# Kernel optimization log

Measured on AMD Instinct MI355X. Metric: run time of the kernel, lower is better.

The kernel has to match this reference:

```python
import jax, jax.numpy as jnp
import numpy as np


def _mamba_branch(xz, conv_w, conv_b, xproj_w, dtproj_w, dtproj_b, A_log, Dp):
    # xz: (b, l, 2*d_inner)
    d_inner, d_state = A_log.shape
    dt_rank = dtproj_w.shape[1]
    k = conv_w.shape[-1]
    x, z = jnp.split(xz, 2, axis=-1)                      # (b, l, d_inner) each
    # depthwise causal conv over the sequence dim (torch pads d_conv-1 then trims to L)
    xc = jax.lax.conv_general_dilated(
        x.transpose(0, 2, 1), conv_w, (1,), [(k - 1, 0)],
        feature_group_count=d_inner,
        dimension_numbers=('NCH', 'OIH', 'NCH'))
    x = jax.nn.silu((xc + conv_b[None, :, None]).transpose(0, 2, 1))  # (b, l, d)
    dbl = x @ xproj_w.T                                   # (b, l, dt_rank + 2*n)
    dt, Bs, Cs = jnp.split(dbl, [dt_rank, dt_rank + d_state], axis=-1)
    delta = jax.nn.softplus(dt @ dtproj_w.T + dtproj_b)   # (b, l, d)
    A = -jnp.exp(A_log)                                   # (d, n), always negative

    def step(h, inp):
        d_t, B_t, u_t, C_t = inp                          # (b,d),(b,n),(b,d),(b,n)
        h = jnp.exp(d_t[..., None] * A) * h + (d_t * u_t)[..., None] * B_t[:, None, :]
        return h, jnp.einsum('bdn,bn->bd', h, C_t)

    h0 = jnp.zeros((x.shape[0], d_inner, d_state), x.dtype)
    _, ys = jax.lax.scan(step, h0,
                         (delta.transpose(1, 0, 2), Bs.transpose(1, 0, 2),
                          x.transpose(1, 0, 2), Cs.transpose(1, 0, 2)))
    y = ys.transpose(1, 0, 2) + x * Dp                    # (b, l, d)
    return y * jax.nn.silu(z)


def setup_inputs() -> dict:
    key = jax.random.key(0)
    ks = jax.random.split(key, 12)
    dim, d_state, d_conv, expand = 256, 16, 4, 2
    d_inner = expand * dim
    dt_rank = dim // 16
    s = 0.02
    r = lambda k, shp: s * jax.random.normal(k, shp, jnp.float32)
    A_init = jnp.log(jnp.tile(jnp.arange(1, d_state + 1, dtype=jnp.float32), (d_inner, 1)))
    dt_bias = jnp.log(jnp.expm1(0.01 * jnp.ones((d_inner,), jnp.float32)))
    return {
        'x': jax.random.normal(ks[0], (8, dim, 64, 64), jnp.float32),
        'ln_w': jnp.ones((dim,), jnp.float32),
        'ln_b': jnp.zeros((dim,), jnp.float32),
        'in_proj_w': r(ks[1], (2 * d_inner, dim)),
        'conv1d_w': r(ks[2], (d_inner, 1, d_conv)),
        'conv1d_b': jnp.zeros((d_inner,), jnp.float32),
        'x_proj_w': r(ks[3], (dt_rank + 2 * d_state, d_inner)),
        'dt_proj_w': r(ks[4], (d_inner, dt_rank)),
        'dt_proj_b': dt_bias,
        'A_log': A_init,
        'D': jnp.ones((d_inner,), jnp.float32),
        'conv1d_b_w': r(ks[5], (d_inner, 1, d_conv)),
        'conv1d_b_b': jnp.zeros((d_inner,), jnp.float32),
        'x_proj_b_w': r(ks[6], (dt_rank + 2 * d_state, d_inner)),
        'dt_proj_b_w': r(ks[7], (d_inner, dt_rank)),
        'dt_proj_b_b': dt_bias,
        'A_b_log': A_init,
        'D_b': jnp.ones((d_inner,), jnp.float32),
        'out_proj_w': r(ks[8], (dim, d_inner)),
    }


def reference(x, ln_w, ln_b, in_proj_w, conv1d_w, conv1d_b, x_proj_w, dt_proj_w,
              dt_proj_b, A_log, D, conv1d_b_w, conv1d_b_b, x_proj_b_w,
              dt_proj_b_w, dt_proj_b_b, A_b_log, D_b, out_proj_w):
    B, C, H, W = x.shape
    xf = x.reshape(B, C, H * W).transpose(0, 2, 1)        # (b, l, c)
    mu = jnp.mean(xf, -1, keepdims=True)
    var = jnp.mean((xf - mu) ** 2, -1, keepdims=True)
    xn = (xf - mu) / jnp.sqrt(var + 1e-5) * ln_w + ln_b   # LayerNorm(dim)
    xz = xn @ in_proj_w.T                                 # (b, l, 2*d_inner)
    y_f = _mamba_branch(xz, conv1d_w, conv1d_b, x_proj_w, dt_proj_w,
                        dt_proj_b, A_log, D)
    y_b = _mamba_branch(xz[:, ::-1, :], conv1d_b_w, conv1d_b_b, x_proj_b_w,
                        dt_proj_b_w, dt_proj_b_b, A_b_log, D_b)[:, ::-1, :]
    out = (y_f + y_b) @ out_proj_w.T                      # (b, l, c)
    return out.transpose(0, 2, 1).reshape(B, C, H, W)
```

## Files before the change

### kernel.cpp

```cpp
#include <hip/hip_runtime.h>
#include <cstdint>
#include <cstddef>

#define L_SEQ   4096
#define NBATCH  8
#define NDIM    256
#define DIN     512
#define NSTATE  16
#define NC_CHUNKS 32
#define CLEN    (L_SEQ / NC_CHUNKS)
#define BLROWS  (NBATCH * L_SEQ)

typedef unsigned short u16;
typedef __attribute__((ext_vector_type(8))) short short8;
typedef __attribute__((ext_vector_type(4))) float f32x4;

#define LOG2E 1.44269504088896340736f

__device__ __forceinline__ u16 f2bf(float f) {
  unsigned u = __float_as_uint(f);
  return (u16)((u + 0x7FFFu + ((u >> 16) & 1u)) >> 16);
}
__device__ __forceinline__ float bf2f(u16 v) {
  return __uint_as_float(((unsigned)v) << 16);
}
__device__ __forceinline__ float exp2fast(float x) {
#if __has_builtin(__builtin_amdgcn_exp2f)
  return __builtin_amdgcn_exp2f(x);
#else
  return exp2f(x);
#endif
}
__device__ __forceinline__ float sigmoid_(float x) {
  return 1.0f / (1.0f + exp2fast(-x * LOG2E));
}
__device__ __forceinline__ float silu_(float x) { return x * sigmoid_(x); }
__device__ __forceinline__ float softplus_(float x) {
  return (x > 15.f) ? x : __logf(1.0f + exp2fast(x * LOG2E));
}

__global__ __launch_bounds__(256) void k_prep(
    const float* __restrict__ in_w, const float* __restrict__ xp_f,
    const float* __restrict__ xp_b, const float* __restrict__ out_w,
    const float* __restrict__ Alog_f, const float* __restrict__ Alog_b,
    u16* __restrict__ wb_in, u16* __restrict__ wb_xp, u16* __restrict__ wb_cat,
    float* __restrict__ a2) {
  int i = blockIdx.x * 256 + threadIdx.x;
  if (i < 1024 * 256) wb_in[i] = f2bf(in_w[i]);
  if (i < 2 * 48 * 512) {
    int d = i / (48 * 512), r = i % (48 * 512);
    wb_xp[i] = f2bf((d ? xp_b : xp_f)[r]);
  }
  if (i < 256 * 1024) {
    int c = i >> 10, k = i & 1023;
    wb_cat[i] = f2bf(out_w[c * 512 + (k & 511)]);
  }
  if (i < 2 * 8192) {
    int d = i >> 13, r = i & 8191;
    a2[i] = -__expf((d ? Alog_b : Alog_f)[r]) * LOG2E;
  }
}

__global__ __launch_bounds__(256) void k_ln(
    const float* __restrict__ x, const float* __restrict__ w,
    const float* __restrict__ bb, u16* __restrict__ xn) {
  __shared__ float tile[256][65];
  __shared__ float red[2][4][64];
  __shared__ float mu_s[64], rs_s[64];
  int b = blockIdx.y, l0 = blockIdx.x * 64;
  int t = threadIdx.x, lane = t & 63, r = t >> 6;
  const float* xb = x + (size_t)b * 256 * L_SEQ;
  for (int cc = 0; cc < 64; ++cc) {
    int c = cc * 4 + r;
    tile[c][lane] = xb[(size_t)c * L_SEQ + l0 + lane];
  }
  __syncthreads();
  float s = 0.f, sq = 0.f;
  for (int c = r * 64; c < r * 64 + 64; ++c) {
    float v = tile[c][lane];
    s += v; sq += v * v;
  }
  red[0][r][lane] = s; red[1][r][lane] = sq;
  __syncthreads();
  if (t < 64) {
    float S = red[0][0][t] + red[0][1][t] + red[0][2][t] + red[0][3][t];
    float Q = red[1][0][t] + red[1][1][t] + red[1][2][t] + red[1][3][t];
    float mu = S * (1.f / 256.f);
    float var = Q * (1.f / 256.f) - mu * mu;
    mu_s[t] = mu;
    rs_s[t] = rsqrtf(var + 1e-5f);
  }
  __syncthreads();
  float wc = w[t], bc = bb[t];
  for (int l = 0; l < 64; ++l) {
    float v = (tile[t][l] - mu_s[l]) * rs_s[l] * wc + bc;
    xn[((size_t)b * L_SEQ + l0 + l) * 256 + t] = f2bf(v);
  }
}

__global__ __launch_bounds__(256) void k_gemm_in(
    const u16* __restrict__ A, const u16* __restrict__ Bm,
    u16* __restrict__ xout, u16* __restrict__ zout) {
  __shared__ u16 lA[128 * 32], lB[128 * 32];
  int mt = blockIdx.x, nt = blockIdx.y;
  int t = threadIdx.x, lane = t & 63, wid = t >> 6;
  int wr = wid >> 1, wc = wid & 1;
  f32x4 acc[4][4] = {};
  const u16* Ab = A + (size_t)mt * 128 * 256;
  const u16* Bb = Bm + (size_t)nt * 128 * 256;
  for (int kt = 0; kt < 8; ++kt) {
    int k0 = kt * 32;
    __syncthreads();
#pragma unroll
    for (int i = 0; i < 2; ++i) {
      int lin = i * 256 + t, row = lin >> 2, kc = lin & 3;
      *(short8*)&lA[lin * 8] = *(const short8*)&Ab[row * 256 + k0 + kc * 8];
      *(short8*)&lB[lin * 8] = *(const short8*)&Bb[row * 256 + k0 + kc * 8];
    }
    __syncthreads();
    short8 av[4], bv[4];
#pragma unroll
    for (int i = 0; i < 4; ++i)
      av[i] = *(const short8*)&lA[(wr * 64 + i * 16 + (lane & 15)) * 32 + (lane >> 4) * 8];
#pragma unroll
    for (int j = 0; j < 4; ++j)
      bv[j] = *(const short8*)&lB[(wc * 64 + j * 16 + (lane & 15)) * 32 + (lane >> 4) * 8];
#pragma unroll
    for (int i = 0; i < 4; ++i)
#pragma unroll
      for (int j = 0; j < 4; ++j)
        acc[i][j] = __builtin_amdgcn_mfma_f32_16x16x32_bf16(av[i], bv[j], acc[i][j], 0, 0, 0);
  }
  int colbase = nt * 128 + wc * 64;
  u16* dst = (colbase < 512) ? xout : zout;
  int cadj = (colbase < 512) ? colbase : colbase - 512;
  size_t rowbase = (size_t)mt * 128 + wr * 64;
#pragma unroll
  for (int i = 0; i < 4; ++i)
#pragma unroll
    for (int j = 0; j < 4; ++j) {
      int c = cadj + j * 16 + (lane & 15);
      size_t rr = rowbase + i * 16 + ((lane >> 4) << 2);
#pragma unroll
      for (int ii = 0; ii < 4; ++ii)
        dst[(rr + ii) * 512 + c] = f2bf(acc[i][j][ii]);
    }
}

__global__ __launch_bounds__(512) void k_conv(
    const u16* __restrict__ xbuf,
    const float* __restrict__ cw_f, const float* __restrict__ cb_f,
    const float* __restrict__ cw_b, const float* __restrict__ cb_b,
    u16* __restrict__ xconv_bf) {
  int d = threadIdx.x;
  int b = blockIdx.y, dir = blockIdx.z;
  int t0 = blockIdx.x * 64;
  const float* cw = (dir ? cw_b : cw_f) + d * 4;
  float w0 = cw[0], w1 = cw[1], w2 = cw[2], w3 = cw[3];
  float bias = (dir ? cb_b : cb_f)[d];
  const u16* xb = xbuf + (size_t)b * L_SEQ * 512 + d;
  u16* ob = xconv_bf + ((size_t)dir * BLROWS + (size_t)b * L_SEQ) * 512 + d;
  float tp0 = 0.f, tp1 = 0.f, tp2 = 0.f;
  if (t0 >= 1) tp2 = bf2f(xb[(size_t)(dir ? (L_SEQ - t0) : (t0 - 1)) * 512]);
  if (t0 >= 2) tp1 = bf2f(xb[(size_t)(dir ? (L_SEQ + 1 - t0) : (t0 - 2)) * 512]);
  if (t0 >= 3) tp0 = bf2f(xb[(size_t)(dir ? (L_SEQ + 2 - t0) : (t0 - 3)) * 512]);
#pragma unroll 4
  for (int tt = t0; tt < t0 + 64; ++tt) {
    int px = dir ? (L_SEQ - 1 - tt) : tt;
    float xin = bf2f(xb[(size_t)px * 512]);
    float u = bias + w0 * tp0 + w1 * tp1 + w2 * tp2 + w3 * xin;
    ob[(size_t)tt * 512] = f2bf(silu_(u));
    tp0 = tp1; tp1 = tp2; tp2 = xin;
  }
}

__global__ __launch_bounds__(256) void k_gemm_xp(
    const u16* __restrict__ xc, const u16* __restrict__ wxp,
    float* __restrict__ dbl) {
  __shared__ u16 lA[128 * 32], lB[48 * 32];
  int mt = blockIdx.x, dir = blockIdx.y;
  int t = threadIdx.x, lane = t & 63, wid = t >> 6;
  const u16* Ab = xc + ((size_t)dir * BLROWS + (size_t)mt * 128) * 512;
  const u16* Bb = wxp + (size_t)dir * 48 * 512;
  float* Ob = dbl + ((size_t)dir * BLROWS + (size_t)mt * 128) * 48;
  f32x4 acc[2][3] = {};
  for (int kt = 0; kt < 16; ++kt) {
    int k0 = kt * 32;
    __syncthreads();
#pragma unroll
    for (int i = 0; i < 2; ++i) {
      int lin = i * 256 + t, row = lin >> 2, kc = lin & 3;
      *(short8*)&lA[lin * 8] = *(const short8*)&Ab[row * 512 + k0 + kc * 8];
    }
    if (t < 192) {
      int row = t >> 2, kc = t & 3;
      *(short8*)&lB[t * 8] = *(const short8*)&Bb[row * 512 + k0 + kc * 8];
    }
    __syncthreads();
    short8 av[2], bv[3];
#pragma unroll
    for (int i = 0; i < 2; ++i)
      av[i] = *(const short8*)&lA[(wid * 32 + i * 16 + (lane & 15)) * 32 + (lane >> 4) * 8];
#pragma unroll
    for (int j = 0; j < 3; ++j)
      bv[j] = *(const short8*)&lB[(j * 16 + (lane & 15)) * 32 + (lane >> 4) * 8];
#pragma unroll
    for (int i = 0; i < 2; ++i)
#pragma unroll
      for (int j = 0; j < 3; ++j)
        acc[i][j] = __builtin_amdgcn_mfma_f32_16x16x32_bf16(av[i], bv[j], acc[i][j], 0, 0, 0);
  }
#pragma unroll
  for (int i = 0; i < 2; ++i)
#pragma unroll
    for (int j = 0; j < 3; ++j) {
      int c = j * 16 + (lane & 15);
      int rr = wid * 32 + i * 16 + ((lane >> 4) << 2);
#pragma unroll
      for (int ii = 0; ii < 4; ++ii)
        Ob[(size_t)(rr + ii) * 48 + c] = acc[i][j][ii];
    }
}

__global__ __launch_bounds__(512, 4) void k_scanA(
    const u16* __restrict__ xbuf, const float* __restrict__ dbl,
    const float* __restrict__ a2buf,
    const float* __restrict__ cw_f, const float* __restrict__ cb_f,
    const float* __restrict__ cw_b, const float* __restrict__ cb_b,
    const float* __restrict__ dtw_f, const float* __restrict__ dtb_f,
    const float* __restrict__ dtw_b, const float* __restrict__ dtb_b,
    float* __restrict__ Pb, float* __restrict__ Hf) {
  int chunk = blockIdx.x, b = blockIdx.y, dir = blockIdx.z;
  int d = threadIdx.x;
  f32x4 a2r[4], w3r[4];
  const f32x4* A2 = (const f32x4*)(a2buf + dir * 8192 + (size_t)d * 16);
  const f32x4* dtw = (const f32x4*)((dir ? dtw_b : dtw_f) + (size_t)d * 16);
#pragma unroll
  for (int q = 0; q < 4; ++q) { a2r[q] = A2[q]; w3r[q] = dtw[q]; }
  const float* cw = (dir ? cw_b : cw_f) + d * 4;
  float w0 = cw[0], w1 = cw[1], w2 = cw[2], w3 = cw[3];
  float cbias = (dir ? cb_b : cb_f)[d];
  float dtbias = (dir ? dtb_b : dtb_f)[d];
  const u16* xb = xbuf + (size_t)b * L_SEQ * 512 + d;
  const float* dbr = dbl + ((size_t)dir * BLROWS + (size_t)b * L_SEQ) * 48;
  int t0 = chunk * CLEN;
  float tp0 = 0.f, tp1 = 0.f, tp2 = 0.f;
  if (t0 >= 1) tp2 = bf2f(xb[(size_t)(dir ? (L_SEQ - t0) : (t0 - 1)) * 512]);
  if (t0 >= 2) tp1 = bf2f(xb[(size_t)(dir ? (L_SEQ + 1 - t0) : (t0 - 2)) * 512]);
  if (t0 >= 3) tp0 = bf2f(xb[(size_t)(dir ? (L_SEQ + 2 - t0) : (t0 - 3)) * 512]);
  f32x4 h[4] = {};
  float S = 0.f;
  for (int tt = t0; tt < t0 + CLEN; ++tt) {
    int px = dir ? (L_SEQ - 1 - tt) : tt;
    float xin = bf2f(xb[(size_t)px * 512]);
    float u = silu_(cbias + w0 * tp0 + w1 * tp1 + w2 * tp2 + w3 * xin);
    tp0 = tp1; tp1 = tp2; tp2 = xin;
    const f32x4* row4 = (const f32x4*)(dbr + (size_t)tt * 48);
    float v0 = 0.f, v1 = 0.f, v2 = 0.f, v3 = 0.f;
#pragma unroll
    for (int q = 0; q < 4; ++q) {
      f32x4 dq = row4[q];
      v0 = fmaf(dq[0], w3r[q][0], v0); v1 = fmaf(dq[1], w3r[q][1], v1);
      v2 = fmaf(dq[2], w3r[q][2], v2); v3 = fmaf(dq[3], w3r[q][3], v3);
    }
    float delta = softplus_(dtbias + ((v0 + v1) + (v2 + v3)));
    S += delta;
    float du = delta * u;
#pragma unroll
    for (int q = 0; q < 4; ++q) {
      f32x4 Bv = row4[4 + q];
#pragma unroll
      for (int j = 0; j < 4; ++j)
        h[q][j] = fmaf(exp2fast(delta * a2r[q][j]), h[q][j], du * Bv[j]);
    }
  }
  size_t base = (((size_t)dir * NBATCH + b) * NC_CHUNKS + chunk) * 8192 + (size_t)d * 16;
#pragma unroll
  for (int q = 0; q < 4; ++q) {
    *(f32x4*)&Hf[base + q * 4] = h[q];
    f32x4 pv;
#pragma unroll
    for (int j = 0; j < 4; ++j) pv[j] = exp2fast(S * a2r[q][j]);
    *(f32x4*)&Pb[base + q * 4] = pv;
  }
}

__global__ __launch_bounds__(512) void k_scanB(
    const float* __restrict__ P, const float* __restrict__ Hf,
    float* __restrict__ Hi) {
  int dir = blockIdx.z, b = blockIdx.y;
  int j = blockIdx.x * 512 + threadIdx.x;
  size_t base0 = (((size_t)dir * NBATCH + b) * NC_CHUNKS) * 8192 + j;
  float h = 0.f;
  for (int c = 0; c < NC_CHUNKS; ++c) {
    size_t idx = base0 + (size_t)c * 8192;
    Hi[idx] = h;
    h = P[idx] * h + Hf[idx];
  }
}

__global__ __launch_bounds__(512, 4) void k_scanC(
    const u16* __restrict__ xbuf, const u16* __restrict__ zbuf,
    const float* __restrict__ dbl, const float* __restrict__ a2buf,
    const float* __restrict__ cw_f, const float* __restrict__ cb_f,
    const float* __restrict__ cw_b, const float* __restrict__ cb_b,
    const float* __restrict__ dtw_f, const float* __restrict__ dtb_f,
    const float* __restrict__ dtw_b, const float* __restrict__ dtb_b,
    const float* __restrict__ D_f, const float* __restrict__ D_b,
    const float* __restrict__ Hi, u16* __restrict__ ycat) {
  int chunk = blockIdx.x, b = blockIdx.y, dir = blockIdx.z;
  int d = threadIdx.x;
  f32x4 a2r[4], w3r[4];
  const f32x4* A2 = (const f32x4*)(a2buf + dir * 8192 + (size_t)d * 16);
  const f32x4* dtw = (const f32x4*)((dir ? dtw_b : dtw_f) + (size_t)d * 16);
#pragma unroll
  for (int q = 0; q < 4; ++q) { a2r[q] = A2[q]; w3r[q] = dtw[q]; }
  const float* cw = (dir ? cw_b : cw_f) + d * 4;
  float w0 = cw[0], w1 = cw[1], w2 = cw[2], w3 = cw[3];
  float cbias = (dir ? cb_b : cb_f)[d];
  float dtbias = (dir ? dtb_b : dtb_f)[d];
  float Dd = (dir ? D_b : D_f)[d];
  const u16* xb = xbuf + (size_t)b * L_SEQ * 512 + d;
  const u16* zb = zbuf + (size_t)b * L_SEQ * 512 + d;
  const float* dbr = dbl + ((size_t)dir * BLROWS + (size_t)b * L_SEQ) * 48;
  u16* yb = ycat + (size_t)b * L_SEQ * 1024 + dir * 512 + d;
  int t0 = chunk * CLEN;
  float tp0 = 0.f, tp1 = 0.f, tp2 = 0.f;
  if (t0 >= 1) tp2 = bf2f(xb[(size_t)(dir ? (L_SEQ - t0) : (t0 - 1)) * 512]);
  if (t0 >= 2) tp1 = bf2f(xb[(size_t)(dir ? (L_SEQ + 1 - t0) : (t0 - 2)) * 512]);
  if (t0 >= 3) tp0 = bf2f(xb[(size_t)(dir ? (L_SEQ + 2 - t0) : (t0 - 3)) * 512]);
  f32x4 h[4];
  size_t hbase = (((size_t)dir * NBATCH + b) * NC_CHUNKS + chunk) * 8192 + (size_t)d * 16;
#pragma unroll
  for (int q = 0; q < 4; ++q) h[q] = *(const f32x4*)&Hi[hbase + q * 4];
  for (int tt = t0; tt < t0 + CLEN; ++tt) {
    int px = dir ? (L_SEQ - 1 - tt) : tt;
    float xin = bf2f(xb[(size_t)px * 512]);
    float u = silu_(cbias + w0 * tp0 + w1 * tp1 + w2 * tp2 + w3 * xin);
    tp0 = tp1; tp1 = tp2; tp2 = xin;
    const f32x4* row4 = (const f32x4*)(dbr + (size_t)tt * 48);
    float v0 = 0.f, v1 = 0.f, v2 = 0.f, v3 = 0.f;
#pragma unroll
    for (int q = 0; q < 4; ++q) {
      f32x4 dq = row4[q];
      v0 = fmaf(dq[0], w3r[q][0], v0); v1 = fmaf(dq[1], w3r[q][1], v1);
      v2 = fmaf(dq[2], w3r[q][2], v2); v3 = fmaf(dq[3], w3r[q][3], v3);
    }
    float delta = softplus_(dtbias + ((v0 + v1) + (v2 + v3)));
    float du = delta * u;
    f32x4 yv = {0.f, 0.f, 0.f, 0.f};
#pragma unroll
    for (int q = 0; q < 4; ++q) {
      f32x4 Bv = row4[4 + q];
      f32x4 Cv = row4[8 + q];
#pragma unroll
      for (int j = 0; j < 4; ++j) {
        h[q][j] = fmaf(exp2fast(delta * a2r[q][j]), h[q][j], du * Bv[j]);
        yv[j] = fmaf(h[q][j], Cv[j], yv[j]);
      }
    }
    float y = ((yv[0] + yv[1]) + (yv[2] + yv[3])) + u * Dd;
    float z = bf2f(zb[(size_t)px * 512]);
    yb[(size_t)px * 1024] = f2bf(y * silu_(z));
  }
}

__global__ __launch_bounds__(256) void k_gemm_out(
    const u16* __restrict__ A, const u16* __restrict__ Bm,
    float* __restrict__ out) {
  __shared__ u16 lA[128 * 32], lB[128 * 32];
  int mt = blockIdx.x, nt = blockIdx.y;
  int t = threadIdx.x, lane = t & 63, wid = t >> 6;
  int wr = wid >> 1, wc = wid & 1;
  f32x4 acc[4][4] = {};
  const u16* Ab = A + (size_t)mt * 128 * 1024;
  const u16* Bb = Bm + (size_t)nt * 128 * 1024;
  for (int kt = 0; kt < 32; ++kt) {
    int k0 = kt * 32;
    __syncthreads();
#pragma unroll
    for (int i = 0; i < 2; ++i) {
      int lin = i * 256 + t, row = lin >> 2, kc = lin & 3;
      *(short8*)&lA[lin * 8] = *(const short8*)&Ab[(size_t)row * 1024 + k0 + kc * 8];
      *(short8*)&lB[lin * 8] = *(const short8*)&Bb[(size_t)row * 1024 + k0 + kc * 8];
    }
    __syncthreads();
    short8 av[4], bv[4];
#pragma unroll
    for (int i = 0; i < 4; ++i)
      av[i] = *(const short8*)&lA[(wr * 64 + i * 16 + (lane & 15)) * 32 + (lane >> 4) * 8];
#pragma unroll
    for (int j = 0; j < 4; ++j)
      bv[j] = *(const short8*)&lB[(wc * 64 + j * 16 + (lane & 15)) * 32 + (lane >> 4) * 8];
#pragma unroll
    for (int i = 0; i < 4; ++i)
#pragma unroll
      for (int j = 0; j < 4; ++j)
        acc[i][j] = __builtin_amdgcn_mfma_f32_16x16x32_bf16(av[i], bv[j], acc[i][j], 0, 0, 0);
  }
#pragma unroll
  for (int i = 0; i < 4; ++i)
#pragma unroll
    for (int j = 0; j < 4; ++j) {
      int c = nt * 128 + wc * 64 + j * 16 + (lane & 15);
      int r0 = mt * 128 + wr * 64 + i * 16 + ((lane >> 4) << 2);
      int b = r0 >> 12, l0 = r0 & 4095;
      float4 val;
      val.x = acc[i][j][0]; val.y = acc[i][j][1];
      val.z = acc[i][j][2]; val.w = acc[i][j][3];
      *(float4*)&out[((size_t)b * 256 + c) * 4096 + l0] = val;
    }
}

extern "C" void kernel_launch(void* const* d_in, const int* in_sizes, int n_in,
                              void* d_out, int out_size, void* d_ws, size_t ws_size,
                              hipStream_t stream) {
  (void)in_sizes; (void)n_in; (void)out_size; (void)ws_size;
  const float* x      = (const float*)d_in[0];
  const float* ln_w   = (const float*)d_in[1];
  const float* ln_b   = (const float*)d_in[2];
  const float* in_w   = (const float*)d_in[3];
  const float* cw_f   = (const float*)d_in[4];
  const float* cb_f   = (const float*)d_in[5];
  const float* xp_f   = (const float*)d_in[6];
  const float* dtw_f  = (const float*)d_in[7];
  const float* dtb_f  = (const float*)d_in[8];
  const float* Alog_f = (const float*)d_in[9];
  const float* D_f    = (const float*)d_in[10];
  const float* cw_b   = (const float*)d_in[11];
  const float* cb_b   = (const float*)d_in[12];
  const float* xp_b   = (const float*)d_in[13];
  const float* dtw_b  = (const float*)d_in[14];
  const float* dtb_b  = (const float*)d_in[15];
  const float* Alog_b = (const float*)d_in[16];
  const float* D_b    = (const float*)d_in[17];
  const float* out_w  = (const float*)d_in[18];

  char* ws = (char*)d_ws;
  size_t off = 0;
  auto alloc = [&](size_t bytes) -> void* {
    void* p = ws + off;
    off += (bytes + 255) & ~(size_t)255;
    return p;
  };
  u16*   xn_bf  = (u16*)  alloc((size_t)BLROWS * 256 * 2);
  u16*   wb_in  = (u16*)  alloc((size_t)1024 * 256 * 2);
  u16*   wb_xp  = (u16*)  alloc((size_t)2 * 48 * 512 * 2);
  u16*   wb_cat = (u16*)  alloc((size_t)256 * 1024 * 2);
  float* a2buf  = (float*)alloc((size_t)2 * 8192 * 4);
  u16*   xbuf   = (u16*)  alloc((size_t)BLROWS * 512 * 2);
  u16*   zbuf   = (u16*)  alloc((size_t)BLROWS * 512 * 2);
  u16*   xconv  = (u16*)  alloc((size_t)2 * BLROWS * 512 * 2);
  float* dblb   = (float*)alloc((size_t)2 * BLROWS * 48 * 4);
  float* Hfbuf  = (float*)alloc((size_t)2 * NBATCH * NC_CHUNKS * 8192 * 4);
  float* Hibuf  = (float*)alloc((size_t)2 * NBATCH * NC_CHUNKS * 8192 * 4);
  float* Pbuf   = (float*)xn_bf;
  u16*   ycat   = xconv;

  hipLaunchKernelGGL(k_prep, dim3(1024), dim3(256), 0, stream,
                     in_w, xp_f, xp_b, out_w, Alog_f, Alog_b,
                     wb_in, wb_xp, wb_cat, a2buf);
  hipLaunchKernelGGL(k_ln, dim3(L_SEQ / 64, NBATCH), dim3(256), 0, stream,
                     x, ln_w, ln_b, xn_bf);
  hipLaunchKernelGGL(k_gemm_in, dim3(BLROWS / 128, 8), dim3(256), 0, stream,
                     xn_bf, wb_in, xbuf, zbuf);
  hipLaunchKernelGGL(k_conv, dim3(L_SEQ / 64, NBATCH, 2), dim3(512), 0, stream,
                     xbuf, cw_f, cb_f, cw_b, cb_b, xconv);
  hipLaunchKernelGGL(k_gemm_xp, dim3(BLROWS / 128, 2), dim3(256), 0, stream,
                     xconv, wb_xp, dblb);
  hipLaunchKernelGGL(k_scanA, dim3(NC_CHUNKS, NBATCH, 2), dim3(512), 0, stream,
                     xbuf, dblb, a2buf, cw_f, cb_f, cw_b, cb_b,
                     dtw_f, dtb_f, dtw_b, dtb_b, Pbuf, Hfbuf);
  hipLaunchKernelGGL(k_scanB, dim3(16, NBATCH, 2), dim3(512), 0, stream,
                     Pbuf, Hfbuf, Hibuf);
  hipLaunchKernelGGL(k_scanC, dim3(NC_CHUNKS, NBATCH, 2), dim3(512), 0, stream,
                     xbuf, zbuf, dblb, a2buf, cw_f, cb_f, cw_b, cb_b,
                     dtw_f, dtb_f, dtw_b, dtb_b, D_f, D_b, Hibuf, ycat);
  hipLaunchKernelGGL(k_gemm_out, dim3(BLROWS / 128, 2), dim3(256), 0, stream,
                     ycat, wb_cat, (float*)d_out);
}
```

Measured before the change: 621.1 us.

## Split scan state across four lanes per channel and reuse precomputed conv output

The chunked scan kernels now give each channel's 16 SSM states to four lanes instead of one thread. The dt projection and the C-weighted output are reduced with cross-lane shuffles, and the grid grows fourfold. The depthwise conv and SiLU are no longer recomputed in the scan; the scan reads the conv buffer already produced for the x-projection GEMM. The output ycat gets its own buffer because xconv must stay alive. This trades more threads and shuffle traffic for less per-thread serial work, fewer registers and higher occupancy.

```diff
diff --git a/kernel.cpp b/kernel.cpp
--- a/kernel.cpp
+++ b/kernel.cpp
@@ -223,66 +223,48 @@
 }
 
 __global__ __launch_bounds__(512, 4) void k_scanA(
-    const u16* __restrict__ xbuf, const float* __restrict__ dbl,
+    const u16* __restrict__ uconv, const float* __restrict__ dbl,
     const float* __restrict__ a2buf,
-    const float* __restrict__ cw_f, const float* __restrict__ cb_f,
-    const float* __restrict__ cw_b, const float* __restrict__ cb_b,
     const float* __restrict__ dtw_f, const float* __restrict__ dtb_f,
     const float* __restrict__ dtw_b, const float* __restrict__ dtb_b,
     float* __restrict__ Pb, float* __restrict__ Hf) {
-  int chunk = blockIdx.x, b = blockIdx.y, dir = blockIdx.z;
-  int d = threadIdx.x;
-  f32x4 a2r[4], w3r[4];
-  const f32x4* A2 = (const f32x4*)(a2buf + dir * 8192 + (size_t)d * 16);
-  const f32x4* dtw = (const f32x4*)((dir ? dtw_b : dtw_f) + (size_t)d * 16);
-#pragma unroll
-  for (int q = 0; q < 4; ++q) { a2r[q] = A2[q]; w3r[q] = dtw[q]; }
-  const float* cw = (dir ? cw_b : cw_f) + d * 4;
-  float w0 = cw[0], w1 = cw[1], w2 = cw[2], w3 = cw[3];
-  float cbias = (dir ? cb_b : cb_f)[d];
+  int chunk = blockIdx.x >> 2, cb = blockIdx.x & 3;
+  int b = blockIdx.y, dir = blockIdx.z;
+  int t = threadIdx.x, wid = t >> 6, lane = t & 63;
+  int ch = lane & 15, grp = lane >> 4;
+  int d = cb * 128 + wid * 16 + ch;
+  f32x4 a2r = *(const f32x4*)(a2buf + dir * 8192 + (size_t)d * 16 + grp * 4);
+  f32x4 w3r = *(const f32x4*)((dir ? dtw_b : dtw_f) + (size_t)d * 16 + grp * 4);
   float dtbias = (dir ? dtb_b : dtb_f)[d];
-  const u16* xb = xbuf + (size_t)b * L_SEQ * 512 + d;
-  const float* dbr = dbl + ((size_t)dir * BLROWS + (size_t)b * L_SEQ) * 48;
+  const u16* ub = uconv + ((size_t)dir * BLROWS + (size_t)b * L_SEQ) * 512 + d;
+  const float* dbr = dbl + ((size_t)dir * BLROWS + (size_t)b * L_SEQ) * 48 + grp * 4;
   int t0 = chunk * CLEN;
-  float tp0 = 0.f, tp1 = 0.f, tp2 = 0.f;
-  if (t0 >= 1) tp2 = bf2f(xb[(size_t)(dir ? (L_SEQ - t0) : (t0 - 1)) * 512]);
-  if (t0 >= 2) tp1 = bf2f(xb[(size_t)(dir ? (L_SEQ + 1 - t0) : (t0 - 2)) * 512]);
-  if (t0 >= 3) tp0 = bf2f(xb[(size_t)(dir ? (L_SEQ + 2 - t0) : (t0 - 3)) * 512]);
-  f32x4 h[4] = {};
+  f32x4 h = {0.f, 0.f, 0.f, 0.f};
   float S = 0.f;
   for (int tt = t0; tt < t0 + CLEN; ++tt) {
-    int px = dir ? (L_SEQ - 1 - tt) : tt;
-    float xin = bf2f(xb[(size_t)px * 512]);
-    float u = silu_(cbias + w0 * tp0 + w1 * tp1 + w2 * tp2 + w3 * xin);
-    tp0 = tp1; tp1 = tp2; tp2 = xin;
-    const f32x4* row4 = (const f32x4*)(dbr + (size_t)tt * 48);
-    float v0 = 0.f, v1 = 0.f, v2 = 0.f, v3 = 0.f;
-#pragma unroll
-    for (int q = 0; q < 4; ++q) {
-      f32x4 dq = row4[q];
-      v0 = fmaf(dq[0], w3r[q][0], v0); v1 = fmaf(dq[1], w3r[q][1], v1);
-      v2 = fmaf(dq[2], w3r[q][2], v2); v3 = fmaf(dq[3], w3r[q][3], v3);
-    }
-    float delta = softplus_(dtbias + ((v0 + v1) + (v2 + v3)));
+    float u = bf2f(ub[(size_t)tt * 512]);
+    f32x4 dq = *(const f32x4*)(dbr + (size_t)tt * 48);
+    f32x4 Bv = *(const f32x4*)(dbr + (size_t)tt * 48 + 16);
+    float part = dq[0] * w3r[0];
+    part = fmaf(dq[1], w3r[1], part);
+    part = fmaf(dq[2], w3r[2], part);
+    part = fmaf(dq[3], w3r[3], part);
+    part += __shfl_xor(part, 16);
+    part += __shfl_xor(part, 32);
+    float delta = softplus_(dtbias + part);
     S += delta;
     float du = delta * u;
 #pragma unroll
-    for (int q = 0; q < 4; ++q) {
-      f32x4 Bv = row4[4 + q];
-#pragma unroll
-      for (int j = 0; j < 4; ++j)
-        h[q][j] = fmaf(exp2fast(delta * a2r[q][j]), h[q][j], du * Bv[j]);
-    }
-  }
-  size_t base = (((size_t)dir * NBATCH + b) * NC_CHUNKS + chunk) * 8192 + (size_t)d * 16;
-#pragma unroll
-  for (int q = 0; q < 4; ++q) {
-    *(f32x4*)&Hf[base + q * 4] = h[q];
-    f32x4 pv;
-#pragma unroll
-    for (int j = 0; j < 4; ++j) pv[j] = exp2fast(S * a2r[q][j]);
-    *(f32x4*)&Pb[base + q * 4] = pv;
-  }
+    for (int j = 0; j < 4; ++j)
+      h[j] = fmaf(exp2fast(delta * a2r[j]), h[j], du * Bv[j]);
+  }
+  size_t base = (((size_t)dir * NBATCH + b) * NC_CHUNKS + chunk) * 8192
+              + (size_t)d * 16 + grp * 4;
+  *(f32x4*)&Hf[base] = h;
+  f32x4 pv;
+#pragma unroll
+  for (int j = 0; j < 4; ++j) pv[j] = exp2fast(S * a2r[j]);
+  *(f32x4*)&Pb[base] = pv;
 }
 
 __global__ __launch_bounds__(512) void k_scanB(
@@ -300,68 +282,56 @@
 }
 
 __global__ __launch_bounds__(512, 4) void k_scanC(
-    const u16* __restrict__ xbuf, const u16* __restrict__ zbuf,
+    const u16* __restrict__ uconv, const u16* __restrict__ zbuf,
     const float* __restrict__ dbl, const float* __restrict__ a2buf,
-    const float* __restrict__ cw_f, const float* __restrict__ cb_f,
-    const float* __restrict__ cw_b, const float* __restrict__ cb_b,
     const float* __restrict__ dtw_f, const float* __restrict__ dtb_f,
     const float* __restrict__ dtw_b, const float* __restrict__ dtb_b,
     const float* __restrict__ D_f, const float* __restrict__ D_b,
     const float* __restrict__ Hi, u16* __restrict__ ycat) {
-  int chunk = blockIdx.x, b = blockIdx.y, dir = blockIdx.z;
-  int d = threadIdx.x;
-  f32x4 a2r[4], w3r[4];
-  const f32x4* A2 = (const f32x4*)(a2buf + dir * 8192 + (size_t)d * 16);
-  const f32x4* dtw = (const f32x4*)((dir ? dtw_b : dtw_f) + (size_t)d * 16);
-#pragma unroll
-  for (int q = 0; q < 4; ++q) { a2r[q] = A2[q]; w3r[q] = dtw[q]; }
-  const float* cw = (dir ? cw_b : cw_f) + d * 4;
-  float w0 = cw[0], w1 = cw[1], w2 = cw[2], w3 = cw[3];
-  float cbias = (dir ? cb_b : cb_f)[d];
+  int chunk = blockIdx.x >> 2, cb = blockIdx.x & 3;
+  int b = blockIdx.y, dir = blockIdx.z;
+  int t = threadIdx.x, wid = t >> 6, lane = t & 63;
+  int ch = lane & 15, grp = lane >> 4;
+  int d = cb * 128 + wid * 16 + ch;
+  f32x4 a2r = *(const f32x4*)(a2buf + dir * 8192 + (size_t)d * 16 + grp * 4);
+  f32x4 w3r = *(const f32x4*)((dir ? dtw_b : dtw_f) + (size_t)d * 16 + grp * 4);
   float dtbias = (dir ? dtb_b : dtb_f)[d];
   float Dd = (dir ? D_b : D_f)[d];
-  const u16* xb = xbuf + (size_t)b * L_SEQ * 512 + d;
+  const u16* ub = uconv + ((size_t)dir * BLROWS + (size_t)b * L_SEQ) * 512 + d;
   const u16* zb = zbuf + (size_t)b * L_SEQ * 512 + d;
-  const float* dbr = dbl + ((size_t)dir * BLROWS + (size_t)b * L_SEQ) * 48;
+  const float* dbr = dbl + ((size_t)dir * BLROWS + (size_t)b * L_SEQ) * 48 + grp * 4;
   u16* yb = ycat + (size_t)b * L_SEQ * 1024 + dir * 512 + d;
   int t0 = chunk * CLEN;
-  float tp0 = 0.f, tp1 = 0.f, tp2 = 0.f;
-  if (t0 >= 1) tp2 = bf2f(xb[(size_t)(dir ? (L_SEQ - t0) : (t0 - 1)) * 512]);
-  if (t0 >= 2) tp1 = bf2f(xb[(size_t)(dir ? (L_SEQ + 1 - t0) : (t0 - 2)) * 512]);
-  if (t0 >= 3) tp0 = bf2f(xb[(size_t)(dir ? (L_SEQ + 2 - t0) : (t0 - 3)) * 512]);
-  f32x4 h[4];
-  size_t hbase = (((size_t)dir * NBATCH + b) * NC_CHUNKS + chunk) * 8192 + (size_t)d * 16;
-#pragma unroll
-  for (int q = 0; q < 4; ++q) h[q] = *(const f32x4*)&Hi[hbase + q * 4];
+  size_t hbase = (((size_t)dir * NBATCH + b) * NC_CHUNKS + chunk) * 8192
+               + (size_t)d * 16 + grp * 4;
+  f32x4 h = *(const f32x4*)&Hi[hbase];
   for (int tt = t0; tt < t0 + CLEN; ++tt) {
     int px = dir ? (L_SEQ - 1 - tt) : tt;
-    float xin = bf2f(xb[(size_t)px * 512]);
-    float u = silu_(cbias + w0 * tp0 + w1 * tp1 + w2 * tp2 + w3 * xin);
-    tp0 = tp1; tp1 = tp2; tp2 = xin;
-    const f32x4* row4 = (const f32x4*)(dbr + (size_t)tt * 48);
-    float v0 = 0.f, v1 = 0.f, v2 = 0.f, v3 = 0.f;
-#pragma unroll
-    for (int q = 0; q < 4; ++q) {
-      f32x4 dq = row4[q];
-      v0 = fmaf(dq[0], w3r[q][0], v0); v1 = fmaf(dq[1], w3r[q][1], v1);
-      v2 = fmaf(dq[2], w3r[q][2], v2); v3 = fmaf(dq[3], w3r[q][3], v3);
-    }
-    float delta = softplus_(dtbias + ((v0 + v1) + (v2 + v3)));
+    float u = bf2f(ub[(size_t)tt * 512]);
+    float z = bf2f(zb[(size_t)px * 512]);
+    f32x4 dq = *(const f32x4*)(dbr + (size_t)tt * 48);
+    f32x4 Bv = *(const f32x4*)(dbr + (size_t)tt * 48 + 16);
+    f32x4 Cv = *(const f32x4*)(dbr + (size_t)tt * 48 + 32);
+    float part = dq[0] * w3r[0];
+    part = fmaf(dq[1], w3r[1], part);
+    part = fmaf(dq[2], w3r[2], part);
+    part = fmaf(dq[3], w3r[3], part);
+    part += __shfl_xor(part, 16);
+    part += __shfl_xor(part, 32);
+    float delta = softplus_(dtbias + part);
     float du = delta * u;
-    f32x4 yv = {0.f, 0.f, 0.f, 0.f};
-#pragma unroll
-    for (int q = 0; q < 4; ++q) {
-      f32x4 Bv = row4[4 + q];
-      f32x4 Cv = row4[8 + q];
-#pragma unroll
-      for (int j = 0; j < 4; ++j) {
-        h[q][j] = fmaf(exp2fast(delta * a2r[q][j]), h[q][j], du * Bv[j]);
-        yv[j] = fmaf(h[q][j], Cv[j], yv[j]);
-      }
-    }
-    float y = ((yv[0] + yv[1]) + (yv[2] + yv[3])) + u * Dd;
-    float z = bf2f(zb[(size_t)px * 512]);
-    yb[(size_t)px * 1024] = f2bf(y * silu_(z));
+    float yp = 0.f;
+#pragma unroll
+    for (int j = 0; j < 4; ++j) {
+      h[j] = fmaf(exp2fast(delta * a2r[j]), h[j], du * Bv[j]);
+      yp = fmaf(h[j], Cv[j], yp);
+    }
+    yp += __shfl_xor(yp, 16);
+    yp += __shfl_xor(yp, 32);
+    if (grp == 0) {
+      float y = yp + u * Dd;
+      yb[(size_t)px * 1024] = f2bf(y * silu_(z));
+    }
   }
 }
 
@@ -454,8 +424,8 @@
   float* dblb   = (float*)alloc((size_t)2 * BLROWS * 48 * 4);
   float* Hfbuf  = (float*)alloc((size_t)2 * NBATCH * NC_CHUNKS * 8192 * 4);
   float* Hibuf  = (float*)alloc((size_t)2 * NBATCH * NC_CHUNKS * 8192 * 4);
+  u16*   ycat   = (u16*)  alloc((size_t)BLROWS * 1024 * 2);
   float* Pbuf   = (float*)xn_bf;
-  u16*   ycat   = xconv;
 
   hipLaunchKernelGGL(k_prep, dim3(1024), dim3(256), 0, stream,
                      in_w, xp_f, xp_b, out_w, Alog_f, Alog_b,
@@ -468,13 +438,13 @@
                      xbuf, cw_f, cb_f, cw_b, cb_b, xconv);
   hipLaunchKernelGGL(k_gemm_xp, dim3(BLROWS / 128, 2), dim3(256), 0, stream,
                      xconv, wb_xp, dblb);
-  hipLaunchKernelGGL(k_scanA, dim3(NC_CHUNKS, NBATCH, 2), dim3(512), 0, stream,
-                     xbuf, dblb, a2buf, cw_f, cb_f, cw_b, cb_b,
+  hipLaunchKernelGGL(k_scanA, dim3(NC_CHUNKS * 4, NBATCH, 2), dim3(512), 0, stream,
+                     xconv, dblb, a2buf,
                      dtw_f, dtb_f, dtw_b, dtb_b, Pbuf, Hfbuf);
   hipLaunchKernelGGL(k_scanB, dim3(16, NBATCH, 2), dim3(512), 0, stream,
                      Pbuf, Hfbuf, Hibuf);
-  hipLaunchKernelGGL(k_scanC, dim3(NC_CHUNKS, NBATCH, 2), dim3(512), 0, stream,
-                     xbuf, zbuf, dblb, a2buf, cw_f, cb_f, cw_b, cb_b,
+  hipLaunchKernelGGL(k_scanC, dim3(NC_CHUNKS * 4, NBATCH, 2), dim3(512), 0, stream,
+                     xconv, zbuf, dblb, a2buf,
                      dtw_f, dtb_f, dtw_b, dtb_b, D_f, D_b, Hibuf, ycat);
   hipLaunchKernelGGL(k_gemm_out, dim3(BLROWS / 128, 2), dim3(256), 0, stream,
                      ycat, wb_cat, (float*)d_out);
```

New measurement: 710.1 us. +14.3%, slower.
